# Kernel optimization log

Measured on AMD Instinct MI355X. Metric: run time of the kernel, lower is better.

Reference implementation:

```python
import jax, jax.numpy as jnp
import numpy as np

# Architecture search space (matches init_kwargs)
IN_DIMS = (512, 768, 1024)
OUT_MULTS = (2, 3, 4)
MAX_IN = max(IN_DIMS)                       # 1024
MAX_OUT = max(IN_DIMS) * max(OUT_MULTS)     # 4096


def _masks():
    # k iterates (i over IN_DIMS, j over OUT_MULTS) in row-major order, matching
    # the original double loop. Slicing weight[:out_dim, :in_dim] then zero-padding
    # to [MAX_OUT, MAX_IN] is equivalent to multiplying by rank-1 mask
    # row_mask[k] (x) col_mask[k].
    out_dims = np.array([m * i for i in IN_DIMS for m in OUT_MULTS])  # [K=9]
    in_dims = np.array([i for i in IN_DIMS for _ in OUT_MULTS])       # [K=9]
    row_mask = (np.arange(MAX_OUT)[None, :] < out_dims[:, None]).astype(np.float32)  # [K, MAX_OUT]
    col_mask = (np.arange(MAX_IN)[None, :] < in_dims[:, None]).astype(np.float32)    # [K, MAX_IN]
    return jnp.asarray(row_mask), jnp.asarray(col_mask)


def setup_inputs() -> dict:
    key = jax.random.key(0)
    k1, k2, k3, k4 = jax.random.split(key, 4)
    x = jax.random.normal(k1, (8, 4096, MAX_IN), dtype=jnp.float32)
    weights = jax.random.uniform(k2, (9,), dtype=jnp.float32)  # mixing coefficients
    W = jax.random.normal(k3, (MAX_OUT, MAX_IN), dtype=jnp.float32) * 0.02  # linear_layer.weight
    b = jax.random.normal(k4, (MAX_OUT,), dtype=jnp.float32) * 0.02         # linear_layer.bias
    return {"x": x, "weights": weights, "W": W, "b": b}


def reference(x, weights, W, b):
    # weights_mix = sum_k weights[k] * pad(W[:o_k, :i_k]) = W * coeff, where
    # coeff[o, i] = sum_k weights[k] * row_mask[k, o] * col_mask[k, i].
    row_mask, col_mask = _masks()
    coeff = jnp.einsum('k,ko,ki->oi', weights, row_mask, col_mask)  # [MAX_OUT, MAX_IN]
    W_mix = W * coeff
    b_mix = b * (weights @ row_mask)                                # [MAX_OUT]
    # F.linear: y = x @ W_mix.T + b_mix
    return jnp.einsum('bsi,oi->bso', x, W_mix) + b_mix
```

## Files before the change

kernel.cpp:

```cpp
#include <hip/hip_runtime.h>

#define KDIM 1024
#define NDIM 4096

typedef __attribute__((ext_vector_type(4))) float f32x4;
typedef __attribute__((ext_vector_type(8))) short s16x8;
typedef __attribute__((ext_vector_type(8))) unsigned short u16x8;

__device__ __forceinline__ unsigned short f2bf(float f) {
    union { float f; unsigned u; } v; v.f = f;
    unsigned r = v.u + 0x7FFFu + ((v.u >> 16) & 1u);
    return (unsigned short)(r >> 16);
}

#define GLDS(gsrc, ldst)                                                        \
    __builtin_amdgcn_global_load_lds(                                           \
        (const __attribute__((address_space(1))) unsigned int*)(gsrc),          \
        (__attribute__((address_space(3))) unsigned int*)(ldst), 16, 0, 0)

#define SBAR() __builtin_amdgcn_s_barrier()
#define VMW(n) asm volatile("s_waitcnt vmcnt(" #n ")" ::: "memory")
#define LGKM0() asm volatile("s_waitcnt lgkmcnt(0)" ::: "memory")

__device__ __forceinline__ void row_coeffs(int o, const float* w,
                                           float& rp0, float& rp1, float& rp2) {
    rp2 = (o < 2048 ? w[6] : 0.f) + (o < 3072 ? w[7] : 0.f) + w[8];
    rp1 = rp2 + (o < 1536 ? w[3] : 0.f) + (o < 2304 ? w[4] : 0.f) + (o < 3072 ? w[5] : 0.f);
    rp0 = rp1 + (o < 1024 ? w[0] : 0.f) + (o < 1536 ? w[1] : 0.f) + (o < 2048 ? w[2] : 0.f);
}

__device__ __forceinline__ float row_bias_coef(int n, const float* w) {
    return (n < 1024 ? w[0] : 0.f) + (n < 1536 ? w[1] : 0.f)
         + (n < 2048 ? w[2] : 0.f) + (n < 1536 ? w[3] : 0.f)
         + (n < 2304 ? w[4] : 0.f) + (n < 3072 ? w[5] : 0.f)
         + (n < 2048 ? w[6] : 0.f) + (n < 3072 ? w[7] : 0.f) + w[8];
}

__global__ __launch_bounds__(256) void prep_x_p(const float* __restrict__ X,
                                                unsigned short* __restrict__ XB,
                                                int nchunks) {
    const int g = blockIdx.x * 256 + threadIdx.x;
    if (g >= nchunks) return;
    const int c   = g & 511;
    const int p   = g >> 9;
    const int kt  = p & 31;
    const int mt  = p >> 5;
    const int row = c >> 2;
    const int kcl = (c & 3) ^ ((row >> 1) & 3);
    const float* src = X + ((size_t)(mt * 128 + row) * KDIM + kt * 32 + kcl * 8);
    f32x4 a = *(const f32x4*)src, b = *(const f32x4*)(src + 4);
    u16x8 o;
    o[0] = f2bf(a[0]); o[1] = f2bf(a[1]); o[2] = f2bf(a[2]); o[3] = f2bf(a[3]);
    o[4] = f2bf(b[0]); o[5] = f2bf(b[1]); o[6] = f2bf(b[2]); o[7] = f2bf(b[3]);
    *(u16x8*)(XB + (size_t)g * 8) = o;
}

__global__ __launch_bounds__(256) void prep_w_p(const float* __restrict__ W,
                                                const float* __restrict__ wts,
                                                unsigned short* __restrict__ WB,
                                                int nchunks) {
    const int g = blockIdx.x * 256 + threadIdx.x;
    if (g >= nchunks) return;
    const int c   = g & 1023;
    const int p   = g >> 10;
    const int kt  = p & 31;
    const int nt  = p >> 5;
    const int row = c >> 2;
    const int kcl = (c & 3) ^ ((row >> 1) & 3);
    float w[9];
#pragma unroll
    for (int k = 0; k < 9; ++k) w[k] = wts[k];
    float rp0, rp1, rp2;
    row_coeffs(nt * 256 + row, w, rp0, rp1, rp2);
    const int i0 = kt * 32 + kcl * 8;
    const float cf = i0 < 512 ? rp0 : (i0 < 768 ? rp1 : rp2);
    const float* src = W + ((size_t)(nt * 256 + row) * KDIM + i0);
    f32x4 a = *(const f32x4*)src, b = *(const f32x4*)(src + 4);
    u16x8 o;
    o[0] = f2bf(a[0] * cf); o[1] = f2bf(a[1] * cf); o[2] = f2bf(a[2] * cf); o[3] = f2bf(a[3] * cf);
    o[4] = f2bf(b[0] * cf); o[5] = f2bf(b[1] * cf); o[6] = f2bf(b[2] * cf); o[7] = f2bf(b[3] * cf);
    *(u16x8*)(WB + (size_t)g * 8) = o;
}

__global__ __launch_bounds__(512, 4) void mlv2_gemm_v10(
    const unsigned short* __restrict__ XB,
    const unsigned short* __restrict__ WB,
    const float* __restrict__ wts,
    const float* __restrict__ bias,
    float* __restrict__ Y)
{
    __shared__ unsigned short LDS[3 * 12288];

    const int tid = (int)threadIdx.x;
    const int l   = tid & 63;
    const int w   = tid >> 6;
    const int wm  = w >> 2;
    const int wn  = w & 3;

    const int bid = (int)blockIdx.x;
    const int xcd = bid & 7;
    const int i   = bid >> 3;
    const int n_tile = xcd * 2 + (i & 1);
    const int m_tile = i >> 1;
    const int m0 = m_tile * 128;
    const int n0 = n_tile * 256;

    const int rl = l & 15;
    const unsigned swz = (unsigned)((l >> 4) ^ ((rl >> 1) & 3));
    unsigned offA[4], offB[4];
#pragma unroll
    for (int m = 0; m < 4; ++m)
        offA[m] = ((unsigned)(wm * 64 + m * 16 + rl) * 4u + swz) * 8u;
#pragma unroll
    for (int n = 0; n < 4; ++n)
        offB[n] = 4096u + ((unsigned)(wn * 64 + n * 16 + rl) * 4u + swz) * 8u;

    const unsigned cA  = (unsigned)(w * 64 + l) * 8u;
    const unsigned cB0 = (unsigned)(w * 128 + l) * 8u;
    const unsigned cB1 = cB0 + 512u;
    const unsigned dA  = (unsigned)(w * 512);
    const unsigned dB0 = 4096u + (unsigned)(w * 1024);
    const unsigned dB1 = dB0 + 512u;

    auto stage = [&](unsigned ob, int kt) {
        const unsigned short* pa = XB + ((size_t)(m_tile * 32 + kt) << 12);
        const unsigned short* pb = WB + ((size_t)(n_tile * 32 + kt) << 13);
        GLDS(pa + cA,  &LDS[ob + dA]);
        GLDS(pb + cB0, &LDS[ob + dB0]);
        GLDS(pb + cB1, &LDS[ob + dB1]);
    };

    f32x4 acc[4][4];
#pragma unroll
    for (int m = 0; m < 4; ++m)
#pragma unroll
        for (int n = 0; n < 4; ++n) acc[m][n] = (f32x4){0.f, 0.f, 0.f, 0.f};

    auto compute = [&](unsigned ob) {
        const unsigned short* base = &LDS[ob];
        s16x8 a[4], b[4];
#pragma unroll
        for (int n = 0; n < 4; ++n) b[n] = *(const s16x8*)(base + offB[n]);
#pragma unroll
        for (int m = 0; m < 4; ++m) a[m] = *(const s16x8*)(base + offA[m]);
        __builtin_amdgcn_s_setprio(1);
#pragma unroll
        for (int m = 0; m < 4; ++m)
#pragma unroll
            for (int n = 0; n < 4; ++n)
                acc[m][n] = __builtin_amdgcn_mfma_f32_16x16x32_bf16(
                    a[m], b[n], acc[m][n], 0, 0, 0);
        __builtin_amdgcn_s_setprio(0);
    };

    unsigned o0 = 0, o1 = 12288, o2 = 24576;
    stage(o0, 0); stage(o1, 1);
    VMW(3);
    SBAR();

    for (int kt = 0; kt < 30; ++kt) {
        stage(o2, kt + 2);
        compute(o0);
        VMW(3); LGKM0(); SBAR();
        const unsigned t_ = o0; o0 = o1; o1 = o2; o2 = t_;
    }
    compute(o0);
    VMW(0); LGKM0(); SBAR();
    compute(o1);

    float w9[9];
#pragma unroll
    for (int k = 0; k < 9; ++k) w9[k] = wts[k];
    const int gmb = m0 + wm * 64 + (l >> 4) * 4;
    const int gnb = n0 + wn * 64 + rl;
#pragma unroll
    for (int n = 0; n < 4; ++n) {
        const int gn = gnb + n * 16;
        const float bc = bias[gn] * row_bias_coef(gn, w9);
#pragma unroll
        for (int m = 0; m < 4; ++m) {
            float* yp = Y + (size_t)(gmb + m * 16) * NDIM + gn;
            yp[0 * NDIM] = acc[m][n][0] + bc;
            yp[1 * NDIM] = acc[m][n][1] + bc;
            yp[2 * NDIM] = acc[m][n][2] + bc;
            yp[3 * NDIM] = acc[m][n][3] + bc;
        }
    }
}

__global__ __launch_bounds__(256, 2) void mlv2_gemm_v1(
    const float* __restrict__ X, const float* __restrict__ wts,
    const float* __restrict__ W, const float* __restrict__ bias,
    float* __restrict__ Y)
{
    __shared__ unsigned short Alds[2][4][128][8];
    __shared__ unsigned short Blds[2][4][128][8];
    const int tid = (int)threadIdx.x;
    const int bid = (int)blockIdx.x;
    const int wg  = (bid & 7) * 1024 + (bid >> 3);
    const int n_tile = wg & 31;
    const int m_tile = wg >> 5;
    float w[9];
#pragma unroll
    for (int k = 0; k < 9; ++k) w[k] = wts[k];
    const int srow = tid >> 1;
    const int scol = (tid & 1) << 4;
    const int kc0  = (tid & 1) << 1;
    const float* xp = X + (size_t)(m_tile * 128 + srow) * KDIM + scol;
    const float* wp = W + (size_t)(n_tile * 128 + srow) * KDIM + scol;
    const int orow = n_tile * 128 + srow;
    float rp0, rp1, rp2;
    row_coeffs(orow, w, rp0, rp1, rp2);
    const int lane = tid & 63, wv = tid >> 6;
    const int frow = lane & 15, kcl = lane >> 4;
    const int arow0 = (wv >> 1) * 64 + frow;
    const int brow0 = (wv & 1) * 64 + frow;
    auto coef = [&](int t) -> float { return t < 16 ? rp0 : (t < 24 ? rp1 : rp2); };
    auto stage_load = [&](int t, f32x4 a[4], f32x4 b[4]) {
        const f32x4* xq = (const f32x4*)(xp + t * 32);
        const f32x4* wq = (const f32x4*)(wp + t * 32);
#pragma unroll
        for (int j = 0; j < 4; ++j) { a[j] = xq[j]; b[j] = wq[j]; }
    };
    auto stage_write = [&](int buf, const f32x4 a[4], const f32x4 b[4], float cf) {
        u16x8 va[2], vb[2];
#pragma unroll
        for (int j = 0; j < 4; ++j)
#pragma unroll
            for (int e = 0; e < 4; ++e) {
                const int idx = j * 4 + e;
                va[idx >> 3][idx & 7] = f2bf(a[j][e]);
                vb[idx >> 3][idx & 7] = f2bf(b[j][e] * cf);
            }
        *(u16x8*)&Alds[buf][kc0    ][srow][0] = va[0];
        *(u16x8*)&Alds[buf][kc0 + 1][srow][0] = va[1];
        *(u16x8*)&Blds[buf][kc0    ][srow][0] = vb[0];
        *(u16x8*)&Blds[buf][kc0 + 1][srow][0] = vb[1];
    };
    f32x4 acc[4][4];
#pragma unroll
    for (int i = 0; i < 4; ++i)
#pragma unroll
        for (int j = 0; j < 4; ++j) acc[i][j] = (f32x4){0.f, 0.f, 0.f, 0.f};
    {
        f32x4 a[4], b[4];
        stage_load(0, a, b);
        stage_write(0, a, b, coef(0));
    }
    __syncthreads();
    const int NT = KDIM / 32;
    int cur = 0;
    for (int t = 0; t < NT; ++t) {
        f32x4 a[4], b[4];
        if (t + 1 < NT) stage_load(t + 1, a, b);
        s16x8 af[4], bf_[4];
#pragma unroll
        for (int i = 0; i < 4; ++i) {
            af[i]  = *(const s16x8*)&Alds[cur][kcl][arow0 + i * 16][0];
            bf_[i] = *(const s16x8*)&Blds[cur][kcl][brow0 + i * 16][0];
        }
#pragma unroll
        for (int i = 0; i < 4; ++i)
#pragma unroll
            for (int j = 0; j < 4; ++j)
                acc[i][j] = __builtin_amdgcn_mfma_f32_16x16x32_bf16(
                    af[i], bf_[j], acc[i][j], 0, 0, 0);
        if (t + 1 < NT) stage_write(cur ^ 1, a, b, coef(t + 1));
        __syncthreads();
        cur ^= 1;
    }
    const int gm0 = m_tile * 128 + (wv >> 1) * 64 + kcl * 4;
    const int gn0 = n_tile * 128 + (wv & 1) * 64 + frow;
#pragma unroll
    for (int j = 0; j < 4; ++j) {
        const int n = gn0 + j * 16;
        const float bc = bias[n] * row_bias_coef(n, w);
#pragma unroll
        for (int i = 0; i < 4; ++i) {
            float* yp = Y + (size_t)(gm0 + i * 16) * NDIM + n;
            yp[0 * NDIM] = acc[i][j][0] + bc;
            yp[1 * NDIM] = acc[i][j][1] + bc;
            yp[2 * NDIM] = acc[i][j][2] + bc;
            yp[3 * NDIM] = acc[i][j][3] + bc;
        }
    }
}

extern "C" void kernel_launch(void* const* d_in, const int* in_sizes, int n_in,
                              void* d_out, int out_size, void* d_ws, size_t ws_size,
                              hipStream_t stream) {
    const float* X    = (const float*)d_in[0];
    const float* wts  = (const float*)d_in[1];
    const float* W    = (const float*)d_in[2];
    const float* bias = (const float*)d_in[3];
    float* Y = (float*)d_out;

    const int M = in_sizes[0] / KDIM;

    const size_t xb_elems = (size_t)M * KDIM;
    const size_t wb_elems = (size_t)NDIM * KDIM;
    const size_t ws_needed = (xb_elems + wb_elems) * sizeof(unsigned short);

    if (ws_size >= ws_needed && (M % 128) == 0) {
        unsigned short* XB = (unsigned short*)d_ws;
        unsigned short* WB = XB + xb_elems;
        const int xchunks = (int)(xb_elems / 8);
        const int wchunks = (int)(wb_elems / 8);
        prep_x_p<<<(xchunks + 255) / 256, 256, 0, stream>>>(X, XB, xchunks);
        prep_w_p<<<(wchunks + 255) / 256, 256, 0, stream>>>(W, wts, WB, wchunks);
        const int grid = (M / 128) * (NDIM / 256);
        mlv2_gemm_v10<<<grid, 512, 0, stream>>>(XB, WB, wts, bias, Y);
    } else {
        const int grid = (M / 128) * (NDIM / 128);
        mlv2_gemm_v1<<<grid, 256, 0, stream>>>(X, wts, W, bias, Y);
    }
}
```

Baseline: 369.1 us.

## Split GEMM k-step into two barrier-synced phases and fuse prep kernels

The main GEMM loop now splits each k-tile into two phases. Each phase issues part of the next tile's global-to-LDS loads, reads half the A fragments, and runs half the MFMAs, with extra barriers and a sched_barrier after the lgkm wait, interleaving memory traffic with compute in a ping-pong style. The two input conversion kernels are merged into one launch to save a kernel launch. The extra barriers per k-step add sync overhead and may serialize waves, in exchange for better overlap of loads and MFMA.

```diff
diff --git a/kernel.cpp b/kernel.cpp
--- a/kernel.cpp
+++ b/kernel.cpp
@@ -20,7 +20,8 @@
 
 #define SBAR() __builtin_amdgcn_s_barrier()
 #define VMW(n) asm volatile("s_waitcnt vmcnt(" #n ")" ::: "memory")
-#define LGKM0() asm volatile("s_waitcnt lgkmcnt(0)" ::: "memory")
+#define LG0()  do { asm volatile("s_waitcnt lgkmcnt(0)" ::: "memory");          \
+                    __builtin_amdgcn_sched_barrier(0); } while (0)
 
 __device__ __forceinline__ void row_coeffs(int o, const float* w,
                                            float& rp0, float& rp1, float& rp2) {
@@ -36,53 +37,52 @@
          + (n < 2048 ? w[6] : 0.f) + (n < 3072 ? w[7] : 0.f) + w[8];
 }
 
-__global__ __launch_bounds__(256) void prep_x_p(const float* __restrict__ X,
+__global__ __launch_bounds__(256) void prep_all(const float* __restrict__ X,
+                                                const float* __restrict__ W,
+                                                const float* __restrict__ wts,
                                                 unsigned short* __restrict__ XB,
-                                                int nchunks) {
+                                                unsigned short* __restrict__ WB,
+                                                int xchunks, int totchunks) {
     const int g = blockIdx.x * 256 + threadIdx.x;
-    if (g >= nchunks) return;
-    const int c   = g & 511;
-    const int p   = g >> 9;
-    const int kt  = p & 31;
-    const int mt  = p >> 5;
-    const int row = c >> 2;
-    const int kcl = (c & 3) ^ ((row >> 1) & 3);
-    const float* src = X + ((size_t)(mt * 128 + row) * KDIM + kt * 32 + kcl * 8);
-    f32x4 a = *(const f32x4*)src, b = *(const f32x4*)(src + 4);
-    u16x8 o;
-    o[0] = f2bf(a[0]); o[1] = f2bf(a[1]); o[2] = f2bf(a[2]); o[3] = f2bf(a[3]);
-    o[4] = f2bf(b[0]); o[5] = f2bf(b[1]); o[6] = f2bf(b[2]); o[7] = f2bf(b[3]);
-    *(u16x8*)(XB + (size_t)g * 8) = o;
-}
-
-__global__ __launch_bounds__(256) void prep_w_p(const float* __restrict__ W,
-                                                const float* __restrict__ wts,
-                                                unsigned short* __restrict__ WB,
-                                                int nchunks) {
-    const int g = blockIdx.x * 256 + threadIdx.x;
-    if (g >= nchunks) return;
-    const int c   = g & 1023;
-    const int p   = g >> 10;
-    const int kt  = p & 31;
-    const int nt  = p >> 5;
-    const int row = c >> 2;
-    const int kcl = (c & 3) ^ ((row >> 1) & 3);
-    float w[9];
-#pragma unroll
-    for (int k = 0; k < 9; ++k) w[k] = wts[k];
-    float rp0, rp1, rp2;
-    row_coeffs(nt * 256 + row, w, rp0, rp1, rp2);
-    const int i0 = kt * 32 + kcl * 8;
-    const float cf = i0 < 512 ? rp0 : (i0 < 768 ? rp1 : rp2);
-    const float* src = W + ((size_t)(nt * 256 + row) * KDIM + i0);
-    f32x4 a = *(const f32x4*)src, b = *(const f32x4*)(src + 4);
-    u16x8 o;
-    o[0] = f2bf(a[0] * cf); o[1] = f2bf(a[1] * cf); o[2] = f2bf(a[2] * cf); o[3] = f2bf(a[3] * cf);
-    o[4] = f2bf(b[0] * cf); o[5] = f2bf(b[1] * cf); o[6] = f2bf(b[2] * cf); o[7] = f2bf(b[3] * cf);
-    *(u16x8*)(WB + (size_t)g * 8) = o;
-}
-
-__global__ __launch_bounds__(512, 4) void mlv2_gemm_v10(
+    if (g >= totchunks) return;
+    if (g < xchunks) {
+        const int c   = g & 511;
+        const int p   = g >> 9;
+        const int kt  = p & 31;
+        const int mt  = p >> 5;
+        const int row = c >> 2;
+        const int kcl = (c & 3) ^ ((row >> 1) & 3);
+        const float* src = X + ((size_t)(mt * 128 + row) * KDIM + kt * 32 + kcl * 8);
+        f32x4 a = *(const f32x4*)src, b = *(const f32x4*)(src + 4);
+        u16x8 o;
+        o[0] = f2bf(a[0]); o[1] = f2bf(a[1]); o[2] = f2bf(a[2]); o[3] = f2bf(a[3]);
+        o[4] = f2bf(b[0]); o[5] = f2bf(b[1]); o[6] = f2bf(b[2]); o[7] = f2bf(b[3]);
+        *(u16x8*)(XB + (size_t)g * 8) = o;
+    } else {
+        const int gw  = g - xchunks;
+        const int c   = gw & 1023;
+        const int p   = gw >> 10;
+        const int kt  = p & 31;
+        const int nt  = p >> 5;
+        const int row = c >> 2;
+        const int kcl = (c & 3) ^ ((row >> 1) & 3);
+        float w[9];
+#pragma unroll
+        for (int k = 0; k < 9; ++k) w[k] = wts[k];
+        float rp0, rp1, rp2;
+        row_coeffs(nt * 256 + row, w, rp0, rp1, rp2);
+        const int i0 = kt * 32 + kcl * 8;
+        const float cf = i0 < 512 ? rp0 : (i0 < 768 ? rp1 : rp2);
+        const float* src = W + ((size_t)(nt * 256 + row) * KDIM + i0);
+        f32x4 a = *(const f32x4*)src, b = *(const f32x4*)(src + 4);
+        u16x8 o;
+        o[0] = f2bf(a[0] * cf); o[1] = f2bf(a[1] * cf); o[2] = f2bf(a[2] * cf); o[3] = f2bf(a[3] * cf);
+        o[4] = f2bf(b[0] * cf); o[5] = f2bf(b[1] * cf); o[6] = f2bf(b[2] * cf); o[7] = f2bf(b[3] * cf);
+        *(u16x8*)(WB + (size_t)gw * 8) = o;
+    }
+}
+
+__global__ __launch_bounds__(512, 4) void mlv2_gemm_v13(
     const unsigned short* __restrict__ XB,
     const unsigned short* __restrict__ WB,
     const float* __restrict__ wts,
@@ -122,51 +122,82 @@
     const unsigned dB0 = 4096u + (unsigned)(w * 1024);
     const unsigned dB1 = dB0 + 512u;
 
-    auto stage = [&](unsigned ob, int kt) {
-        const unsigned short* pa = XB + ((size_t)(m_tile * 32 + kt) << 12);
-        const unsigned short* pb = WB + ((size_t)(n_tile * 32 + kt) << 13);
-        GLDS(pa + cA,  &LDS[ob + dA]);
-        GLDS(pb + cB0, &LDS[ob + dB0]);
-        GLDS(pb + cB1, &LDS[ob + dB1]);
-    };
-
     f32x4 acc[4][4];
 #pragma unroll
     for (int m = 0; m < 4; ++m)
 #pragma unroll
         for (int n = 0; n < 4; ++n) acc[m][n] = (f32x4){0.f, 0.f, 0.f, 0.f};
 
-    auto compute = [&](unsigned ob) {
-        const unsigned short* base = &LDS[ob];
-        s16x8 a[4], b[4];
-#pragma unroll
-        for (int n = 0; n < 4; ++n) b[n] = *(const s16x8*)(base + offB[n]);
-#pragma unroll
-        for (int m = 0; m < 4; ++m) a[m] = *(const s16x8*)(base + offA[m]);
+    s16x8 bfr[4], af2[2];
+
+    auto phaseA = [&](unsigned ob_rd, unsigned ob_st, int kt2, bool st) {
+        if (st) {
+            const unsigned short* pa = XB + ((size_t)(m_tile * 32 + kt2) << 12);
+            const unsigned short* pb = WB + ((size_t)(n_tile * 32 + kt2) << 13);
+            GLDS(pa + cA,  &LDS[ob_st + dA]);
+            GLDS(pb + cB0, &LDS[ob_st + dB0]);
+        }
+        const unsigned short* base = &LDS[ob_rd];
+#pragma unroll
+        for (int n = 0; n < 4; ++n) bfr[n] = *(const s16x8*)(base + offB[n]);
+        af2[0] = *(const s16x8*)(base + offA[0]);
+        af2[1] = *(const s16x8*)(base + offA[1]);
+        SBAR();
+        LG0();
         __builtin_amdgcn_s_setprio(1);
 #pragma unroll
-        for (int m = 0; m < 4; ++m)
+        for (int m = 0; m < 2; ++m)
 #pragma unroll
             for (int n = 0; n < 4; ++n)
                 acc[m][n] = __builtin_amdgcn_mfma_f32_16x16x32_bf16(
-                    a[m], b[n], acc[m][n], 0, 0, 0);
+                    af2[m], bfr[n], acc[m][n], 0, 0, 0);
+        __builtin_amdgcn_s_setprio(0);
+        SBAR();
+    };
+    auto phaseB = [&](unsigned ob_rd, unsigned ob_st, int kt2, bool st) {
+        if (st) {
+            const unsigned short* pb = WB + ((size_t)(n_tile * 32 + kt2) << 13);
+            GLDS(pb + cB1, &LDS[ob_st + dB1]);
+        }
+        const unsigned short* base = &LDS[ob_rd];
+        af2[0] = *(const s16x8*)(base + offA[2]);
+        af2[1] = *(const s16x8*)(base + offA[3]);
+        SBAR();
+        LG0();
+        __builtin_amdgcn_s_setprio(1);
+#pragma unroll
+        for (int m = 0; m < 2; ++m)
+#pragma unroll
+            for (int n = 0; n < 4; ++n)
+                acc[m + 2][n] = __builtin_amdgcn_mfma_f32_16x16x32_bf16(
+                    af2[m], bfr[n], acc[m + 2][n], 0, 0, 0);
         __builtin_amdgcn_s_setprio(0);
     };
 
     unsigned o0 = 0, o1 = 12288, o2 = 24576;
-    stage(o0, 0); stage(o1, 1);
+    {
+        const unsigned short* pa0 = XB + ((size_t)(m_tile * 32 + 0) << 12);
+        const unsigned short* pb0 = WB + ((size_t)(n_tile * 32 + 0) << 13);
+        GLDS(pa0 + cA, &LDS[o0 + dA]); GLDS(pb0 + cB0, &LDS[o0 + dB0]); GLDS(pb0 + cB1, &LDS[o0 + dB1]);
+        const unsigned short* pa1 = XB + ((size_t)(m_tile * 32 + 1) << 12);
+        const unsigned short* pb1 = WB + ((size_t)(n_tile * 32 + 1) << 13);
+        GLDS(pa1 + cA, &LDS[o1 + dA]); GLDS(pb1 + cB0, &LDS[o1 + dB0]); GLDS(pb1 + cB1, &LDS[o1 + dB1]);
+    }
     VMW(3);
     SBAR();
 
     for (int kt = 0; kt < 30; ++kt) {
-        stage(o2, kt + 2);
-        compute(o0);
-        VMW(3); LGKM0(); SBAR();
+        phaseA(o0, o2, kt + 2, true);
+        phaseB(o0, o2, kt + 2, true);
+        VMW(3); SBAR();
         const unsigned t_ = o0; o0 = o1; o1 = o2; o2 = t_;
     }
-    compute(o0);
-    VMW(0); LGKM0(); SBAR();
-    compute(o1);
+    phaseA(o0, 0, 0, false);
+    phaseB(o0, 0, 0, false);
+    VMW(0); SBAR();
+    const unsigned tl = o0; o0 = o1; o1 = o2; o2 = tl;
+    phaseA(o0, 0, 0, false);
+    phaseB(o0, 0, 0, false);
 
     float w9[9];
 #pragma unroll
@@ -304,12 +335,12 @@
     if (ws_size >= ws_needed && (M % 128) == 0) {
         unsigned short* XB = (unsigned short*)d_ws;
         unsigned short* WB = XB + xb_elems;
-        const int xchunks = (int)(xb_elems / 8);
-        const int wchunks = (int)(wb_elems / 8);
-        prep_x_p<<<(xchunks + 255) / 256, 256, 0, stream>>>(X, XB, xchunks);
-        prep_w_p<<<(wchunks + 255) / 256, 256, 0, stream>>>(W, wts, WB, wchunks);
+        const int xchunks   = (int)(xb_elems / 8);
+        const int totchunks = xchunks + (int)(wb_elems / 8);
+        prep_all<<<(totchunks + 255) / 256, 256, 0, stream>>>(X, W, wts, XB, WB,
+                                                              xchunks, totchunks);
         const int grid = (M / 128) * (NDIM / 256);
-        mlv2_gemm_v10<<<grid, 512, 0, stream>>>(XB, WB, wts, bias, Y);
+        mlv2_gemm_v13<<<grid, 512, 0, stream>>>(XB, WB, wts, bias, Y);
     } else {
         const int grid = (M / 128) * (NDIM / 128);
         mlv2_gemm_v1<<<grid, 256, 0, stream>>>(X, wts, W, bias, Y);
```

New measurement: 368.3 us (median of 2 runs). Within noise of the previous version (-0.2%).
